# Kernel optimization log

Measured on AMD Instinct MI355X. Metric: run time of the kernel, lower is better.

## Reference

```python
import jax, jax.numpy as jnp
import numpy as np

DIM_IN = 1024
DIM_QK = 1024
DIM_V = 1024


def setup_inputs() -> dict:
    key = jax.random.key(0)
    ks = jax.random.split(key, 8)
    s = DIM_IN ** -0.5
    return {
        "x": jax.random.normal(ks[0], (16, 2048, DIM_IN), dtype=jnp.float32),
        "encoder_output": jax.random.normal(ks[1], (16, 2048, DIM_IN), dtype=jnp.float32),
        "W_q": jax.random.normal(ks[2], (DIM_IN, DIM_QK), dtype=jnp.float32) * s,
        "b_q": jnp.zeros((DIM_QK,), dtype=jnp.float32),
        "W_k": jax.random.normal(ks[3], (DIM_IN, DIM_QK), dtype=jnp.float32) * s,
        "b_k": jnp.zeros((DIM_QK,), dtype=jnp.float32),
        "W_v": jax.random.normal(ks[4], (DIM_IN, DIM_V), dtype=jnp.float32) * s,
        "b_v": jnp.zeros((DIM_V,), dtype=jnp.float32),
    }


def reference(x, encoder_output, W_q, b_q, W_k, b_k, W_v, b_v):
    # Q: [B, Lq, Dqk]; K, V: [B, Lk, Dqk/Dv]
    Q = x @ W_q + b_q
    K = encoder_output @ W_k + b_k
    V = encoder_output @ W_v + b_v
    # attn_scores: [B, Lq, Lk], scaled by 1/sqrt(Dqk)
    scores = jnp.einsum("bqd,bkd->bqk", Q, K) * (K.shape[-1] ** -0.5)
    weights = jax.nn.softmax(scores, axis=-1)
    H = jnp.einsum("bqk,bkv->bqv", weights, V)  # [B, Lq, Dv]
    return H
```

## Files before the change

kernel.cpp:

```cpp
#include <hip/hip_runtime.h>

typedef _Float16 f16;
typedef __attribute__((ext_vector_type(4))) _Float16 f16x4;
typedef __attribute__((ext_vector_type(8))) _Float16 f16x8;
typedef __attribute__((ext_vector_type(4))) float f32x4;

#define MFMA16(a, b, c) __builtin_amdgcn_mfma_f32_16x16x32_f16(a, b, c, 0, 0, 0)

__device__ __forceinline__ void gll16(const void* g, void* l) {
    __builtin_amdgcn_global_load_lds(
        (const __attribute__((address_space(1))) unsigned int*)g,
        (__attribute__((address_space(3))) unsigned int*)l, 16, 0, 0);
}

#define BAR() __builtin_amdgcn_s_barrier()
#define LGKM(n) do { asm volatile("s_waitcnt lgkmcnt(" #n ")" ::: "memory"); \
                     __builtin_amdgcn_sched_barrier(0); } while (0)
#define VMC(n)  do { asm volatile("s_waitcnt vmcnt(" #n ")" ::: "memory"); \
                     __builtin_amdgcn_sched_barrier(0); } while (0)

__global__ __launch_bounds__(256) void cvt_f16(
    const float* __restrict__ in, f16* __restrict__ out)
{
    const size_t i = ((size_t)blockIdx.x * 256 + threadIdx.x) * 8;
    float4 a = *(const float4*)(in + i);
    float4 b = *(const float4*)(in + i + 4);
    f16x8 o;
    o[0] = (f16)a.x; o[1] = (f16)a.y; o[2] = (f16)a.z; o[3] = (f16)a.w;
    o[4] = (f16)b.x; o[5] = (f16)b.y; o[6] = (f16)b.z; o[7] = (f16)b.w;
    *(f16x8*)(out + i) = o;
}

__global__ __launch_bounds__(256) void prep_weights(
    const float* __restrict__ Wq, const float* __restrict__ Wk,
    const float* __restrict__ Wv, f16* __restrict__ Wt)
{
    __shared__ float tile[32][33];
    const float* W = blockIdx.z == 0 ? Wq : (blockIdx.z == 1 ? Wk : Wv);
    f16* dst = Wt + (size_t)blockIdx.z * 1024 * 1024;
    const int tx = threadIdx.x & 31, ty = threadIdx.x >> 5;
    const int n0 = blockIdx.x * 32, k0 = blockIdx.y * 32;
#pragma unroll
    for (int i = 0; i < 4; i++)
        tile[ty + i * 8][tx] = W[(size_t)(k0 + ty + i * 8) * 1024 + n0 + tx];
    __syncthreads();
#pragma unroll
    for (int i = 0; i < 4; i++)
        dst[(size_t)(n0 + ty + i * 8) * 1024 + k0 + tx] = (f16)tile[tx][ty + i * 8];
}

template <int KD, int EPI>
__global__ __launch_bounds__(512, 2) void gemm8(
    const f16* __restrict__ Ab, const f16* __restrict__ Bb,
    const float* __restrict__ b0, const float* __restrict__ b1, float scale,
    void* __restrict__ C0, void* __restrict__ C1, float* __restrict__ aux,
    size_t strA, size_t strB, size_t strC, int ldc, int nbx, int nby)
{
    __shared__ f16 shA[2][256 * 64];
    __shared__ f16 shB[2][256 * 64];

    int id = blockIdx.x;
    {
        const int chunk = (int)gridDim.x >> 3;
        id = (id & 7) * chunk + (id >> 3);
    }
    const int by = id % nby;
    const int r2 = id / nby;
    const int bx = r2 % nbx;
    const int z  = r2 / nbx;
    const int bm = bx * 256, bn = by * 256;

    const f16* A = Ab + (size_t)z * strA;
    const f16* B = Bb + (size_t)z * strB;

    const int t = threadIdx.x, lane = t & 63, wid = t >> 6;
    const int wr = wid >> 2, wc = wid & 3;
    const int fr = lane & 15, kb = (lane >> 4) * 16;
    const int sw = (fr & 7) << 4;

    const int lsr = lane >> 3;
    const int lsc = ((lane & 7) * 16) ^ (lsr << 4);
    const int a_  = wid * 8;
    const int bq_ = (wid >> 2) * 64 + (wid & 3) * 8;
    const f16* aT = A + (size_t)(bm + lsr) * KD + (lsc >> 1);
    const f16* bT = B + (size_t)(bn + lsr) * KD + (lsc >> 1);

#define STAGE(d, kt)                                                          \
    do {                                                                      \
        const f16* As_ = aT + (size_t)(kt) * 64;                              \
        const f16* Bs_ = bT + (size_t)(kt) * 64;                              \
        f16* da_ = &shA[d][0];                                                \
        f16* db_ = &shB[d][0];                                                \
        gll16(As_ + (size_t)(a_)*KD,        da_ + (a_)*64);                   \
        gll16(As_ + (size_t)(128 + a_)*KD,  da_ + (128 + a_)*64);             \
        gll16(As_ + (size_t)(64 + a_)*KD,   da_ + (64 + a_)*64);              \
        gll16(As_ + (size_t)(192 + a_)*KD,  da_ + (192 + a_)*64);             \
        gll16(Bs_ + (size_t)(bq_)*KD,       db_ + (bq_)*64);                  \
        gll16(Bs_ + (size_t)(128 + bq_)*KD, db_ + (128 + bq_)*64);            \
        gll16(Bs_ + (size_t)(32 + bq_)*KD,  db_ + (32 + bq_)*64);             \
        gll16(Bs_ + (size_t)(160 + bq_)*KD, db_ + (160 + bq_)*64);            \
    } while (0)

    f16x8 af[2][2][4];
    f16x8 bf[2][2][2];
    f32x4 acc[8][4] = {};

#define LDA(mh)                                                               \
    _Pragma("unroll") for (int kk_ = 0; kk_ < 2; ++kk_)                       \
    _Pragma("unroll") for (int i_ = 0; i_ < 4; ++i_)                          \
        af[mh][kk_][i_] = *(const f16x8*)(sAc +                               \
            (wr * 128 + (mh) * 64 + i_ * 16 + fr) * 128 +                     \
            (((kk_ << 6) | kb) ^ sw));

#define LDB(nh)                                                               \
    _Pragma("unroll") for (int kk_ = 0; kk_ < 2; ++kk_)                       \
    _Pragma("unroll") for (int j_ = 0; j_ < 2; ++j_)                          \
        bf[nh][kk_][j_] = *(const f16x8*)(sBc +                               \
            (wc * 64 + (nh) * 32 + j_ * 16 + fr) * 128 +                      \
            (((kk_ << 6) | kb) ^ sw));

#define MM(mh, nh)                                                            \
    __builtin_amdgcn_s_setprio(1);                                            \
    _Pragma("unroll") for (int kk_ = 0; kk_ < 2; ++kk_)                       \
    _Pragma("unroll") for (int i_ = 0; i_ < 4; ++i_)                          \
    _Pragma("unroll") for (int j_ = 0; j_ < 2; ++j_)                          \
        acc[(mh) * 4 + i_][(nh) * 2 + j_] =                                   \
            MFMA16(af[mh][kk_][i_], bf[nh][kk_][j_],                          \
                   acc[(mh) * 4 + i_][(nh) * 2 + j_]);                        \
    __builtin_amdgcn_s_setprio(0);

    constexpr int NT = KD / 64;

    STAGE(0, 0);

    for (int ti = 0; ti < NT; ++ti) {
        const int c = ti & 1;
        const char* sAc = (const char*)&shA[c][0];
        const char* sBc = (const char*)&shB[c][0];
        if (ti + 1 < NT) {
            STAGE(c ^ 1, ti + 1);
            VMC(8);
        } else {
            VMC(0);
        }
        BAR();
        LDA(0); LDB(0); LDB(1); LDA(1);
        LGKM(8);
        MM(0, 0); MM(0, 1);
        LGKM(0);
        MM(1, 1); MM(1, 0);
        BAR();
    }

    const int fc = lane & 15, rq = (lane >> 4) * 4;

    if constexpr (EPI == 2) {
        BAR();
        float* part = (float*)&shA[0][0];
        f16* Sp = (f16*)C0 + (size_t)z * strC;
#pragma unroll
        for (int mi = 0; mi < 8; ++mi)
#pragma unroll
            for (int r = 0; r < 4; ++r) {
                const int rl = wr * 128 + mi * 16 + rq + r;
                float ps = 0.f;
#pragma unroll
                for (int nj = 0; nj < 4; ++nj) {
                    const int col = bn + wc * 64 + nj * 16 + fc;
                    f16 eh = (f16)__expf(acc[mi][nj][r]);
                    ps += (float)eh;
                    Sp[(size_t)(bm + rl) * ldc + col] = eh;
                }
#pragma unroll
                for (int o = 1; o < 16; o <<= 1) ps += __shfl_xor(ps, o);
                if (fc == 0) part[rl * 4 + wc] = ps;
            }
        BAR();
        if (t < 256) {
            const float4 p4 = *(const float4*)(part + t * 4);
            aux[((size_t)z * 2048 + bm + t) * 8 + by] = p4.x + p4.y + p4.z + p4.w;
        }
        return;
    }

#pragma unroll
    for (int nj = 0; nj < 4; ++nj) {
        const int col = bn + wc * 64 + nj * 16 + fc;
        float bv_ = 0.f;
        if constexpr (EPI == 0) bv_ = b0[col];
        if constexpr (EPI == 1) bv_ = (col < 1024) ? b0[col] : b1[col - 1024];
#pragma unroll
        for (int mi = 0; mi < 8; ++mi) {
            if constexpr (EPI == 1) {
                if (col >= 1024) {
                    const int rowb = bm + wr * 128 + mi * 16 + rq;
                    f16x4 q;
#pragma unroll
                    for (int r = 0; r < 4; ++r) q[r] = (f16)(acc[mi][nj][r] + bv_);
                    f16* Cp = (f16*)C1 + (size_t)(rowb >> 11) * 2048 * 1024 +
                              (size_t)(col - 1024) * 2048;
                    *(f16x4*)&Cp[rowb & 2047] = q;
                    continue;
                }
            }
#pragma unroll
            for (int r = 0; r < 4; ++r) {
                const int row = bm + wr * 128 + mi * 16 + rq + r;
                float v = acc[mi][nj][r];
                if constexpr (EPI == 0) v = (v + bv_) * scale;
                if constexpr (EPI == 1) v = v + bv_;
                if constexpr (EPI == 3) v *= aux[(size_t)z * 2048 + row];
                if constexpr (EPI == 0) {
                    ((f16*)C0)[(size_t)row * ldc + col] = (f16)v;
                } else if constexpr (EPI == 1) {
                    ((f16*)C0)[(size_t)row * 1024 + col] = (f16)v;
                } else {
                    ((float*)C0 + (size_t)z * strC)[(size_t)row * ldc + col] = v;
                }
            }
        }
    }
#undef STAGE
#undef LDA
#undef LDB
#undef MM
}

__global__ __launch_bounds__(256) void rowinv_k(
    const float* __restrict__ part, float* __restrict__ inv)
{
    const int q = blockIdx.x * 256 + threadIdx.x;
    const float4* p = (const float4*)(part + (size_t)q * 8);
    const float4 a = p[0], b = p[1];
    inv[q] = 1.0f / (a.x + a.y + a.z + a.w + b.x + b.y + b.z + b.w);
}

extern "C" void kernel_launch(void* const* d_in, const int* in_sizes, int n_in,
                              void* d_out, int out_size, void* d_ws, size_t ws_size,
                              hipStream_t stream)
{
    const float* x   = (const float*)d_in[0];
    const float* enc = (const float*)d_in[1];
    const float* Wq  = (const float*)d_in[2];
    const float* bq  = (const float*)d_in[3];
    const float* Wk  = (const float*)d_in[4];
    const float* bk  = (const float*)d_in[5];
    const float* Wv  = (const float*)d_in[6];
    const float* bv  = (const float*)d_in[7];

    const size_t TOK = (size_t)16 * 2048;
    f16* Qh = (f16*)d_ws;
    f16* Kh = Qh + TOK * 1024;
    f16* Vt = Kh + TOK * 1024;
    f16* Wt = Vt + TOK * 1024;
    f16* S  = Wt + (size_t)3 * 1024 * 1024;
    f16* Xh = S;
    f16* Eh = S + TOK * 1024;
    float* Ppart = (float*)Wt;
    float* Rinv  = Ppart + TOK * 8;

    cvt_f16<<<16384, 256, 0, stream>>>(x,   Xh);
    cvt_f16<<<16384, 256, 0, stream>>>(enc, Eh);

    prep_weights<<<dim3(32, 32, 3), 256, 0, stream>>>(Wq, Wk, Wv, Wt);

    gemm8<1024, 0><<<512, 512, 0, stream>>>(
        Xh, Wt, bq, nullptr, 0.03125f, Qh, nullptr, nullptr,
        0, 0, 0, 1024, 128, 4);

    gemm8<1024, 1><<<1024, 512, 0, stream>>>(
        Eh, Wt + (size_t)1024 * 1024, bk, bv, 1.0f, Kh, Vt, nullptr,
        0, 0, 0, 1024, 128, 8);

    gemm8<1024, 2><<<1024, 512, 0, stream>>>(
        Qh, Kh, nullptr, nullptr, 1.0f, S, nullptr, Ppart,
        (size_t)2048 * 1024, (size_t)2048 * 1024, (size_t)2048 * 2048, 2048, 8, 8);

    rowinv_k<<<128, 256, 0, stream>>>(Ppart, Rinv);

    gemm8<2048, 3><<<512, 512, 0, stream>>>(
        S, Vt, nullptr, nullptr, 1.0f, d_out, nullptr, Rinv,
        (size_t)2048 * 2048, (size_t)1024 * 2048, (size_t)2048 * 1024, 1024, 8, 4);
}
```

Baseline: 707.5 us.

## Interleave split global-to-LDS prefetch quarters with MFMA phases in GEMM loop

```diff
diff --git a/kernel.cpp b/kernel.cpp
--- a/kernel.cpp
+++ b/kernel.cpp
@@ -85,21 +85,22 @@
     const f16* aT = A + (size_t)(bm + lsr) * KD + (lsc >> 1);
     const f16* bT = B + (size_t)(bn + lsr) * KD + (lsc >> 1);
 
-#define STAGE(d, kt)                                                          \
-    do {                                                                      \
-        const f16* As_ = aT + (size_t)(kt) * 64;                              \
-        const f16* Bs_ = bT + (size_t)(kt) * 64;                              \
-        f16* da_ = &shA[d][0];                                                \
-        f16* db_ = &shB[d][0];                                                \
+#define STG_A0(d, kt) do {                                                    \
+        const f16* As_ = aT + (size_t)(kt) * 64; f16* da_ = &shA[d][0];       \
         gll16(As_ + (size_t)(a_)*KD,        da_ + (a_)*64);                   \
-        gll16(As_ + (size_t)(128 + a_)*KD,  da_ + (128 + a_)*64);             \
+        gll16(As_ + (size_t)(128 + a_)*KD,  da_ + (128 + a_)*64); } while (0)
+#define STG_A1(d, kt) do {                                                    \
+        const f16* As_ = aT + (size_t)(kt) * 64; f16* da_ = &shA[d][0];       \
         gll16(As_ + (size_t)(64 + a_)*KD,   da_ + (64 + a_)*64);              \
-        gll16(As_ + (size_t)(192 + a_)*KD,  da_ + (192 + a_)*64);             \
+        gll16(As_ + (size_t)(192 + a_)*KD,  da_ + (192 + a_)*64); } while (0)
+#define STG_B0(d, kt) do {                                                    \
+        const f16* Bs_ = bT + (size_t)(kt) * 64; f16* db_ = &shB[d][0];       \
         gll16(Bs_ + (size_t)(bq_)*KD,       db_ + (bq_)*64);                  \
-        gll16(Bs_ + (size_t)(128 + bq_)*KD, db_ + (128 + bq_)*64);            \
+        gll16(Bs_ + (size_t)(128 + bq_)*KD, db_ + (128 + bq_)*64); } while (0)
+#define STG_B1(d, kt) do {                                                    \
+        const f16* Bs_ = bT + (size_t)(kt) * 64; f16* db_ = &shB[d][0];       \
         gll16(Bs_ + (size_t)(32 + bq_)*KD,  db_ + (32 + bq_)*64);             \
-        gll16(Bs_ + (size_t)(160 + bq_)*KD, db_ + (160 + bq_)*64);            \
-    } while (0)
+        gll16(Bs_ + (size_t)(160 + bq_)*KD, db_ + (160 + bq_)*64); } while (0)
 
     f16x8 af[2][2][4];
     f16x8 bf[2][2][2];
@@ -131,25 +132,28 @@
 
     constexpr int NT = KD / 64;
 
-    STAGE(0, 0);
+    STG_A0(0, 0); STG_B0(0, 0); STG_B1(0, 0); STG_A1(0, 0);
+    VMC(4);
+    BAR();
 
     for (int ti = 0; ti < NT; ++ti) {
         const int c = ti & 1;
+        const int n = c ^ 1;
+        const int kn = ti + 1;
+        const bool pf = (kn < NT);
         const char* sAc = (const char*)&shA[c][0];
         const char* sBc = (const char*)&shB[c][0];
-        if (ti + 1 < NT) {
-            STAGE(c ^ 1, ti + 1);
-            VMC(8);
-        } else {
-            VMC(0);
-        }
-        BAR();
-        LDA(0); LDB(0); LDB(1); LDA(1);
-        LGKM(8);
-        MM(0, 0); MM(0, 1);
-        LGKM(0);
-        MM(1, 1); MM(1, 0);
-        BAR();
+        LDA(0); LDB(0);
+        if (pf) { STG_A0(n, kn); VMC(4); } else { VMC(2); }
+        BAR(); LGKM(0); MM(0, 0); BAR();
+        LDB(1);
+        if (pf) { STG_B0(n, kn); VMC(4); } else { VMC(0); }
+        BAR(); LGKM(0); MM(0, 1); BAR();
+        LDA(1);
+        if (pf) STG_B1(n, kn);
+        BAR(); LGKM(0); MM(1, 1); BAR();
+        if (pf) { STG_A1(n, kn); VMC(4); }
+        BAR(); MM(1, 0); BAR();
     }
 
     const int fc = lane & 15, rq = (lane >> 4) * 4;
@@ -220,7 +224,10 @@
             }
         }
     }
-#undef STAGE
+#undef STG_A0
+#undef STG_A1
+#undef STG_B0
+#undef STG_B1
 #undef LDA
 #undef LDB
 #undef MM
```

Result: faster. 657.5 us (-7.1%).

## Replace 256x256 double-buffered GEMM with simpler 128x128 single-buffered kernel

Applied to the files above, without the earlier changes.

```diff
diff --git a/kernel.cpp b/kernel.cpp
--- a/kernel.cpp
+++ b/kernel.cpp
@@ -12,12 +12,6 @@
         (const __attribute__((address_space(1))) unsigned int*)g,
         (__attribute__((address_space(3))) unsigned int*)l, 16, 0, 0);
 }
-
-#define BAR() __builtin_amdgcn_s_barrier()
-#define LGKM(n) do { asm volatile("s_waitcnt lgkmcnt(" #n ")" ::: "memory"); \
-                     __builtin_amdgcn_sched_barrier(0); } while (0)
-#define VMC(n)  do { asm volatile("s_waitcnt vmcnt(" #n ")" ::: "memory"); \
-                     __builtin_amdgcn_sched_barrier(0); } while (0)
 
 __global__ __launch_bounds__(256) void cvt_f16(
     const float* __restrict__ in, f16* __restrict__ out)
@@ -50,14 +44,14 @@
 }
 
 template <int KD, int EPI>
-__global__ __launch_bounds__(512, 2) void gemm8(
+__global__ __launch_bounds__(256, 3) void gemm97(
     const f16* __restrict__ Ab, const f16* __restrict__ Bb,
     const float* __restrict__ b0, const float* __restrict__ b1, float scale,
     void* __restrict__ C0, void* __restrict__ C1, float* __restrict__ aux,
     size_t strA, size_t strB, size_t strC, int ldc, int nbx, int nby)
 {
-    __shared__ f16 shA[2][256 * 64];
-    __shared__ f16 shB[2][256 * 64];
+    __shared__ f16 shA[128 * 64];
+    __shared__ f16 shB[128 * 64];
 
     int id = blockIdx.x;
     {
@@ -68,101 +62,65 @@
     const int r2 = id / nby;
     const int bx = r2 % nbx;
     const int z  = r2 / nbx;
-    const int bm = bx * 256, bn = by * 256;
+    const int bm = bx * 128, bn = by * 128;
 
     const f16* A = Ab + (size_t)z * strA;
     const f16* B = Bb + (size_t)z * strB;
 
     const int t = threadIdx.x, lane = t & 63, wid = t >> 6;
-    const int wr = wid >> 2, wc = wid & 3;
+    const int wr = wid >> 1, wc = wid & 1;
     const int fr = lane & 15, kb = (lane >> 4) * 16;
     const int sw = (fr & 7) << 4;
 
-    const int lsr = lane >> 3;
-    const int lsc = ((lane & 7) * 16) ^ (lsr << 4);
-    const int a_  = wid * 8;
-    const int bq_ = (wid >> 2) * 64 + (wid & 3) * 8;
-    const f16* aT = A + (size_t)(bm + lsr) * KD + (lsc >> 1);
-    const f16* bT = B + (size_t)(bn + lsr) * KD + (lsc >> 1);
-
-#define STAGE(d, kt)                                                          \
-    do {                                                                      \
-        const f16* As_ = aT + (size_t)(kt) * 64;                              \
-        const f16* Bs_ = bT + (size_t)(kt) * 64;                              \
-        f16* da_ = &shA[d][0];                                                \
-        f16* db_ = &shB[d][0];                                                \
-        gll16(As_ + (size_t)(a_)*KD,        da_ + (a_)*64);                   \
-        gll16(As_ + (size_t)(128 + a_)*KD,  da_ + (128 + a_)*64);             \
-        gll16(As_ + (size_t)(64 + a_)*KD,   da_ + (64 + a_)*64);              \
-        gll16(As_ + (size_t)(192 + a_)*KD,  da_ + (192 + a_)*64);             \
-        gll16(Bs_ + (size_t)(bq_)*KD,       db_ + (bq_)*64);                  \
-        gll16(Bs_ + (size_t)(128 + bq_)*KD, db_ + (128 + bq_)*64);            \
-        gll16(Bs_ + (size_t)(32 + bq_)*KD,  db_ + (32 + bq_)*64);             \
-        gll16(Bs_ + (size_t)(160 + bq_)*KD, db_ + (160 + bq_)*64);            \
-    } while (0)
-
-    f16x8 af[2][2][4];
-    f16x8 bf[2][2][2];
-    f32x4 acc[8][4] = {};
-
-#define LDA(mh)                                                               \
-    _Pragma("unroll") for (int kk_ = 0; kk_ < 2; ++kk_)                       \
-    _Pragma("unroll") for (int i_ = 0; i_ < 4; ++i_)                          \
-        af[mh][kk_][i_] = *(const f16x8*)(sAc +                               \
-            (wr * 128 + (mh) * 64 + i_ * 16 + fr) * 128 +                     \
-            (((kk_ << 6) | kb) ^ sw));
-
-#define LDB(nh)                                                               \
-    _Pragma("unroll") for (int kk_ = 0; kk_ < 2; ++kk_)                       \
-    _Pragma("unroll") for (int j_ = 0; j_ < 2; ++j_)                          \
-        bf[nh][kk_][j_] = *(const f16x8*)(sBc +                               \
-            (wc * 64 + (nh) * 32 + j_ * 16 + fr) * 128 +                      \
-            (((kk_ << 6) | kb) ^ sw));
-
-#define MM(mh, nh)                                                            \
-    __builtin_amdgcn_s_setprio(1);                                            \
-    _Pragma("unroll") for (int kk_ = 0; kk_ < 2; ++kk_)                       \
-    _Pragma("unroll") for (int i_ = 0; i_ < 4; ++i_)                          \
-    _Pragma("unroll") for (int j_ = 0; j_ < 2; ++j_)                          \
-        acc[(mh) * 4 + i_][(nh) * 2 + j_] =                                   \
-            MFMA16(af[mh][kk_][i_], bf[nh][kk_][j_],                          \
-                   acc[(mh) * 4 + i_][(nh) * 2 + j_]);                        \
-    __builtin_amdgcn_s_setprio(0);
+    const int srow = t >> 3;
+    const int scb  = ((t & 7) * 16) ^ ((srow & 7) << 4);
+    const f16* aT0 = A + (size_t)(bm + srow) * KD + (scb >> 1);
+    const f16* bT0 = B + (size_t)(bn + srow) * KD + (scb >> 1);
+    f16* aD = shA + wid * 512;
+    f16* bD = shB + wid * 512;
+
+    f32x4 acc[4][4] = {};
+    const char* sA = (const char*)shA;
+    const char* sB = (const char*)shB;
 
     constexpr int NT = KD / 64;
-
-    STAGE(0, 0);
-
-    for (int ti = 0; ti < NT; ++ti) {
-        const int c = ti & 1;
-        const char* sAc = (const char*)&shA[c][0];
-        const char* sBc = (const char*)&shB[c][0];
-        if (ti + 1 < NT) {
-            STAGE(c ^ 1, ti + 1);
-            VMC(8);
-        } else {
-            VMC(0);
-        }
-        BAR();
-        LDA(0); LDB(0); LDB(1); LDA(1);
-        LGKM(8);
-        MM(0, 0); MM(0, 1);
-        LGKM(0);
-        MM(1, 1); MM(1, 0);
-        BAR();
+    for (int kt = 0; kt < NT; ++kt) {
+#pragma unroll
+        for (int i = 0; i < 4; ++i) {
+            gll16(aT0 + (size_t)(i * 32) * KD + kt * 64, aD + i * 2048);
+            gll16(bT0 + (size_t)(i * 32) * KD + kt * 64, bD + i * 2048);
+        }
+        __syncthreads();
+#pragma unroll
+        for (int kk = 0; kk < 2; ++kk) {
+            f16x8 af[4], bf[4];
+#pragma unroll
+            for (int i = 0; i < 4; ++i)
+                af[i] = *(const f16x8*)(sA + (wr * 64 + i * 16 + fr) * 128 +
+                                        (((kk << 6) | kb) ^ sw));
+#pragma unroll
+            for (int j = 0; j < 4; ++j)
+                bf[j] = *(const f16x8*)(sB + (wc * 64 + j * 16 + fr) * 128 +
+                                        (((kk << 6) | kb) ^ sw));
+#pragma unroll
+            for (int i = 0; i < 4; ++i)
+#pragma unroll
+                for (int j = 0; j < 4; ++j)
+                    acc[i][j] = MFMA16(af[i], bf[j], acc[i][j]);
+        }
+        __syncthreads();
     }
 
     const int fc = lane & 15, rq = (lane >> 4) * 4;
 
     if constexpr (EPI == 2) {
-        BAR();
-        float* part = (float*)&shA[0][0];
+        float* part = (float*)shA;
         f16* Sp = (f16*)C0 + (size_t)z * strC;
 #pragma unroll
-        for (int mi = 0; mi < 8; ++mi)
+        for (int mi = 0; mi < 4; ++mi)
 #pragma unroll
             for (int r = 0; r < 4; ++r) {
-                const int rl = wr * 128 + mi * 16 + rq + r;
+                const int rl = wr * 64 + mi * 16 + rq + r;
                 float ps = 0.f;
 #pragma unroll
                 for (int nj = 0; nj < 4; ++nj) {
@@ -173,12 +131,12 @@
                 }
 #pragma unroll
                 for (int o = 1; o < 16; o <<= 1) ps += __shfl_xor(ps, o);
-                if (fc == 0) part[rl * 4 + wc] = ps;
+                if (fc == 0) part[rl * 2 + wc] = ps;
             }
-        BAR();
-        if (t < 256) {
-            const float4 p4 = *(const float4*)(part + t * 4);
-            aux[((size_t)z * 2048 + bm + t) * 8 + by] = p4.x + p4.y + p4.z + p4.w;
+        __syncthreads();
+        if (t < 128) {
+            const float2 p2 = *(const float2*)(part + t * 2);
+            aux[((size_t)z * 2048 + bm + t) * 16 + by] = p2.x + p2.y;
         }
         return;
     }
@@ -190,10 +148,10 @@
         if constexpr (EPI == 0) bv_ = b0[col];
         if constexpr (EPI == 1) bv_ = (col < 1024) ? b0[col] : b1[col - 1024];
 #pragma unroll
-        for (int mi = 0; mi < 8; ++mi) {
+        for (int mi = 0; mi < 4; ++mi) {
             if constexpr (EPI == 1) {
                 if (col >= 1024) {
-                    const int rowb = bm + wr * 128 + mi * 16 + rq;
+                    const int rowb = bm + wr * 64 + mi * 16 + rq;
                     f16x4 q;
 #pragma unroll
                     for (int r = 0; r < 4; ++r) q[r] = (f16)(acc[mi][nj][r] + bv_);
@@ -205,7 +163,7 @@
             }
 #pragma unroll
             for (int r = 0; r < 4; ++r) {
-                const int row = bm + wr * 128 + mi * 16 + rq + r;
+                const int row = bm + wr * 64 + mi * 16 + rq + r;
                 float v = acc[mi][nj][r];
                 if constexpr (EPI == 0) v = (v + bv_) * scale;
                 if constexpr (EPI == 1) v = v + bv_;
@@ -220,19 +178,20 @@
             }
         }
     }
-#undef STAGE
-#undef LDA
-#undef LDB
-#undef MM
 }
 
 __global__ __launch_bounds__(256) void rowinv_k(
     const float* __restrict__ part, float* __restrict__ inv)
 {
     const int q = blockIdx.x * 256 + threadIdx.x;
-    const float4* p = (const float4*)(part + (size_t)q * 8);
-    const float4 a = p[0], b = p[1];
-    inv[q] = 1.0f / (a.x + a.y + a.z + a.w + b.x + b.y + b.z + b.w);
+    const float4* p = (const float4*)(part + (size_t)q * 16);
+    float s = 0.f;
+#pragma unroll
+    for (int i = 0; i < 4; ++i) {
+        const float4 a = p[i];
+        s += a.x + a.y + a.z + a.w;
+    }
+    inv[q] = 1.0f / s;
 }
 
 extern "C" void kernel_launch(void* const* d_in, const int* in_sizes, int n_in,
@@ -257,28 +216,28 @@
     f16* Xh = S;
     f16* Eh = S + TOK * 1024;
     float* Ppart = (float*)Wt;
-    float* Rinv  = Ppart + TOK * 8;
+    float* Rinv  = Ppart + TOK * 16;
 
     cvt_f16<<<16384, 256, 0, stream>>>(x,   Xh);
     cvt_f16<<<16384, 256, 0, stream>>>(enc, Eh);
 
     prep_weights<<<dim3(32, 32, 3), 256, 0, stream>>>(Wq, Wk, Wv, Wt);
 
-    gemm8<1024, 0><<<512, 512, 0, stream>>>(
+    gemm97<1024, 0><<<2048, 256, 0, stream>>>(
         Xh, Wt, bq, nullptr, 0.03125f, Qh, nullptr, nullptr,
-        0, 0, 0, 1024, 128, 4);
-
-    gemm8<1024, 1><<<1024, 512, 0, stream>>>(
+        0, 0, 0, 1024, 256, 8);
+
+    gemm97<1024, 1><<<4096, 256, 0, stream>>>(
         Eh, Wt + (size_t)1024 * 1024, bk, bv, 1.0f, Kh, Vt, nullptr,
-        0, 0, 0, 1024, 128, 8);
-
-    gemm8<1024, 2><<<1024, 512, 0, stream>>>(
+        0, 0, 0, 1024, 256, 16);
+
+    gemm97<1024, 2><<<4096, 256, 0, stream>>>(
         Qh, Kh, nullptr, nullptr, 1.0f, S, nullptr, Ppart,
-        (size_t)2048 * 1024, (size_t)2048 * 1024, (size_t)2048 * 2048, 2048, 8, 8);
+        (size_t)2048 * 1024, (size_t)2048 * 1024, (size_t)2048 * 2048, 2048, 16, 16);
 
     rowinv_k<<<128, 256, 0, stream>>>(Ppart, Rinv);
 
-    gemm8<2048, 3><<<512, 512, 0, stream>>>(
+    gemm97<2048, 3><<<2048, 256, 0, stream>>>(
         S, Vt, nullptr, nullptr, 1.0f, d_out, nullptr, Rinv,
-        (size_t)2048 * 2048, (size_t)1024 * 2048, (size_t)2048 * 1024, 1024, 8, 4);
-}
+        (size_t)2048 * 2048, (size_t)1024 * 2048, (size_t)2048 * 1024, 1024, 16, 8);
+}
```

After: 663.6 us. -6.2%, faster.
